# Kernel optimization log

Hardware: AMD Instinct MI355X
Metric: run time of the kernel (lower is better)

## Reference

```python
import jax, jax.numpy as jnp
import numpy as np


def setup_inputs() -> dict:
    key = jax.random.key(0)
    k1, k2, k3 = jax.random.split(key, 3)
    N, C, Nf, W, H = 8, 256, 16, 28, 28
    l = jax.random.normal(k1, (N, C, Nf, W, H), dtype=jnp.float32)
    g = jax.random.normal(k2, (N, C, 1, 1, 1), dtype=jnp.float32)
    # 1x1x1 Conv3d(in=C, out=1, bias=False) weight collapses to a length-C vector
    w = jax.random.normal(k3, (C,), dtype=jnp.float32) * (1.0 / np.sqrt(C))
    return {"l": l, "g": g, "w": w}


def reference(l, g, w):
    # l: [N,C,Nf,W,H], g broadcastable to l, w: [C]
    N, C, Nf, W, H = l.shape
    # compatibility score: channel dot-product (1x1x1 conv, out_channels=1)
    c = jnp.einsum('ncfwh,c->nfwh', l + g, w)                      # [N,Nf,W,H]
    # softmax over the spatial dims (W*H) per frame, normalize_attn=True
    a = jax.nn.softmax(c.reshape(N, Nf, W * H), axis=-1)           # [N,Nf,WH]
    a = a.reshape(N, Nf, W, H)
    # attention-weighted spatial sum pooling -> [N,C,Nf]
    g_out = jnp.einsum('nfwh,ncfwh->ncf', a, l)
    # module returns raw compatibility map (pre-softmax) squeezed, and pooled g
    return (c, g_out)
```

## Files before the change

### kernel.cpp

```cpp
#include <hip/hip_runtime.h>
#include <math.h>

constexpr int N_ = 8, C_ = 256, F_ = 16, WH_ = 784;
constexpr int CH_STRIDE = F_ * WH_;
constexpr int COUT_SZ = N_ * F_ * WH_;
constexpr int QP = 196;
constexpr int TILE = 28;
constexpr int NT = 7;
constexpr int LSTR = 36;
constexpr int F4PT = TILE / 4;
constexpr int SOFF = 512 * C_;

__device__ inline float wave_reduce_sum(float v) {
#pragma unroll
  for (int o = 32; o > 0; o >>= 1) v += __shfl_down(v, o, 64);
  return v;
}

__global__ __launch_bounds__(1024, 8) void fused_kernel(
    const float* __restrict__ l, const float* __restrict__ g,
    const float* __restrict__ w, float* __restrict__ out,
    float* __restrict__ ws) {
  __shared__ float buf[C_ * LSTR];
  __shared__ float w_s[C_];
  __shared__ float e_s[TILE];
  __shared__ float red_s[16];
  __shared__ float gb_s;

  const int bid = blockIdx.x;
  const int nf = bid >> 2, qh = bid & 3;
  const int n = nf >> 4, f = nf & 15;
  const int tid = threadIdx.x;
  const int lane = tid & 63, wv = tid >> 6;

  if (tid < C_) w_s[tid] = w[tid];
  float gv = (tid < C_) ? g[n * C_ + tid] * w[tid] : 0.f;
  gv = wave_reduce_sum(gv);
  if (lane == 0) red_s[wv] = gv;
  __syncthreads();
  if (tid == 0) {
    float s = 0.f;
#pragma unroll
    for (int i = 0; i < 16; ++i) s += red_s[i];
    gb_s = s;
  }
  __syncthreads();
  const float gb = gb_s;

  const int idx0 = tid;
  const int c0s = idx0 / F4PT, j0 = idx0 - c0s * F4PT;
  const int og0 = c0s * CH_STRIDE + (j0 << 2);
  const int ol0 = c0s * LSTR + (j0 << 2);
  const int idx1 = 1024 + tid;
  const int c1s = idx1 / F4PT, j1 = idx1 - c1s * F4PT;
  const int og1 = c1s * CH_STRIDE + (j1 << 2);
  const int ol1 = c1s * LSTR + (j1 << 2);
  const bool a1 = (tid < 768);
  const size_t gbase =
      (size_t)n * (C_ * CH_STRIDE) + (size_t)f * WH_ + qh * QP;

  const int p16 = tid >> 4, s16 = tid & 15;
  const int gc = tid >> 2, q = tid & 3;

  float gacc = 0.f;
  float s_part = 0.f;

  for (int t = 0; t < NT; ++t) {
    {
      const float* lp = l + gbase + t * TILE;
      const float4 v0 = *reinterpret_cast<const float4*>(lp + og0);
      if (a1) {
        const float4 v1 = *reinterpret_cast<const float4*>(lp + og1);
        *reinterpret_cast<float4*>(&buf[ol1]) = v1;
      }
      *reinterpret_cast<float4*>(&buf[ol0]) = v0;
    }
    __syncthreads();

    if (tid < TILE * 16) {
      float acc = 0.f;
#pragma unroll
      for (int k = 0; k < 16; ++k) {
        const int c = s16 + (k << 4);
        acc = fmaf(buf[c * LSTR + p16], w_s[c], acc);
      }
      acc += __shfl_down(acc, 8, 64);
      acc += __shfl_down(acc, 4, 64);
      acc += __shfl_down(acc, 2, 64);
      acc += __shfl_down(acc, 1, 64);
      if (s16 == 0) {
        const float cp = acc + gb;
        out[nf * WH_ + qh * QP + t * TILE + p16] = cp;
        const float e = __expf(cp);
        e_s[p16] = e;
        s_part += e;
      }
    }
    __syncthreads();

    {
      const int pb = q * 7;
#pragma unroll
      for (int j = 0; j < 7; ++j)
        gacc = fmaf(buf[gc * LSTR + pb + j], e_s[pb + j], gacc);
    }
    __syncthreads();
  }

  gacc += __shfl_down(gacc, 2, 64);
  gacc += __shfl_down(gacc, 1, 64);
  if (q == 0) ws[bid * C_ + gc] = gacc;

  float sp = wave_reduce_sum(s_part);
  if (lane == 0) red_s[wv] = sp;
  __syncthreads();
  if (tid == 0) {
    float ssum = 0.f;
#pragma unroll
    for (int i = 0; i < 16; ++i) ssum += red_s[i];
    ws[SOFF + bid] = ssum;
  }
}

__global__ __launch_bounds__(1024) void combine_kernel(
    float* __restrict__ out, const float* __restrict__ ws) {
  const int tg = blockIdx.x * 1024 + threadIdx.x;
  const int nf = tg >> 8, c = tg & 255;
  const int n = nf >> 4, f = nf & 15;
  const int b0 = nf << 2;
  const float G = ws[(b0 + 0) * C_ + c] + ws[(b0 + 1) * C_ + c] +
                  ws[(b0 + 2) * C_ + c] + ws[(b0 + 3) * C_ + c];
  const float S = ws[SOFF + b0] + ws[SOFF + b0 + 1] +
                  ws[SOFF + b0 + 2] + ws[SOFF + b0 + 3];
  out[COUT_SZ + (size_t)(n * C_ + c) * F_ + f] = G / S;
}

extern "C" void kernel_launch(void* const* d_in, const int* in_sizes, int n_in,
                              void* d_out, int out_size, void* d_ws,
                              size_t ws_size, hipStream_t stream) {
  const float* l = (const float*)d_in[0];
  const float* g = (const float*)d_in[1];
  const float* w = (const float*)d_in[2];
  float* out = (float*)d_out;
  float* ws = (float*)d_ws;
  fused_kernel<<<dim3(4 * N_ * F_), dim3(1024), 0, stream>>>(l, g, w, out, ws);
  combine_kernel<<<dim3(32), dim3(1024), 0, stream>>>(out, ws);
}
```

Measured before the change: 160.6 us.

## Double-buffer tiles with asynchronous global-to-LDS loads

Replaces the register-staged global-to-shared copy with `__builtin_amdgcn_global_load_lds` direct-to-LDS loads into two unpadded tile buffers. The next tile is prefetched while the current one is being reduced, so global memory latency overlaps with compute instead of stalling every iteration. The first tile is issued before the `g`·`w` bias reduction so that latency is hidden too. One barrier is replaced by a manual waitcnt plus barrier. In exchange the kernel uses more LDS and drops the row padding. Correctness now depends on the DMA writes being complete before the barrier that follows them.

```diff
diff --git a/kernel.cpp b/kernel.cpp
--- a/kernel.cpp
+++ b/kernel.cpp
@@ -7,8 +7,8 @@
 constexpr int QP = 196;
 constexpr int TILE = 28;
 constexpr int NT = 7;
-constexpr int LSTR = 36;
 constexpr int F4PT = TILE / 4;
+constexpr int TILE_F = C_ * TILE;
 constexpr int SOFF = 512 * C_;
 
 __device__ inline float wave_reduce_sum(float v) {
@@ -17,11 +17,18 @@
   return v;
 }
 
+__device__ inline void gload16(const float* gp, float* lp) {
+  __builtin_amdgcn_global_load_lds(
+      (const __attribute__((address_space(1))) void*)gp,
+      (__attribute__((address_space(3))) void*)lp, 16, 0, 0);
+}
+
 __global__ __launch_bounds__(1024, 8) void fused_kernel(
     const float* __restrict__ l, const float* __restrict__ g,
     const float* __restrict__ w, float* __restrict__ out,
     float* __restrict__ ws) {
-  __shared__ float buf[C_ * LSTR];
+  __shared__ float bufA[TILE_F];
+  __shared__ float bufB[TILE_F];
   __shared__ float w_s[C_];
   __shared__ float e_s[TILE];
   __shared__ float red_s[16];
@@ -32,6 +39,23 @@
   const int n = nf >> 4, f = nf & 15;
   const int tid = threadIdx.x;
   const int lane = tid & 63, wv = tid >> 6;
+
+  const int c0 = tid / F4PT, j0 = tid - c0 * F4PT;
+  const int og0 = c0 * CH_STRIDE + (j0 << 2);
+  const int idx1 = 1024 + tid;
+  const int c1 = idx1 / F4PT, j1 = idx1 - c1 * F4PT;
+  const int og1 = c1 * CH_STRIDE + (j1 << 2);
+  const bool a1 = (tid < 768);
+  const int l0 = wv << 8;
+  const int l1 = 4096 + (wv << 8);
+  const size_t gbase =
+      (size_t)n * (C_ * CH_STRIDE) + (size_t)f * WH_ + qh * QP;
+
+  {
+    const float* lp = l + gbase;
+    gload16(lp + og0, &bufA[l0]);
+    if (a1) gload16(lp + og1, &bufA[l1]);
+  }
 
   if (tid < C_) w_s[tid] = w[tid];
   float gv = (tid < C_) ? g[n * C_ + tid] * w[tid] : 0.f;
@@ -47,42 +71,27 @@
   __syncthreads();
   const float gb = gb_s;
 
-  const int idx0 = tid;
-  const int c0s = idx0 / F4PT, j0 = idx0 - c0s * F4PT;
-  const int og0 = c0s * CH_STRIDE + (j0 << 2);
-  const int ol0 = c0s * LSTR + (j0 << 2);
-  const int idx1 = 1024 + tid;
-  const int c1s = idx1 / F4PT, j1 = idx1 - c1s * F4PT;
-  const int og1 = c1s * CH_STRIDE + (j1 << 2);
-  const int ol1 = c1s * LSTR + (j1 << 2);
-  const bool a1 = (tid < 768);
-  const size_t gbase =
-      (size_t)n * (C_ * CH_STRIDE) + (size_t)f * WH_ + qh * QP;
-
   const int p16 = tid >> 4, s16 = tid & 15;
   const int gc = tid >> 2, q = tid & 3;
 
+  float* cur = bufA;
+  float* nxt = bufB;
   float gacc = 0.f;
   float s_part = 0.f;
 
   for (int t = 0; t < NT; ++t) {
-    {
-      const float* lp = l + gbase + t * TILE;
-      const float4 v0 = *reinterpret_cast<const float4*>(lp + og0);
-      if (a1) {
-        const float4 v1 = *reinterpret_cast<const float4*>(lp + og1);
-        *reinterpret_cast<float4*>(&buf[ol1]) = v1;
-      }
-      *reinterpret_cast<float4*>(&buf[ol0]) = v0;
+    if (t + 1 < NT) {
+      const float* lp = l + gbase + (t + 1) * TILE;
+      gload16(lp + og0, &nxt[l0]);
+      if (a1) gload16(lp + og1, &nxt[l1]);
     }
-    __syncthreads();
 
     if (tid < TILE * 16) {
       float acc = 0.f;
 #pragma unroll
       for (int k = 0; k < 16; ++k) {
         const int c = s16 + (k << 4);
-        acc = fmaf(buf[c * LSTR + p16], w_s[c], acc);
+        acc = fmaf(cur[c * TILE + p16], w_s[c], acc);
       }
       acc += __shfl_down(acc, 8, 64);
       acc += __shfl_down(acc, 4, 64);
@@ -96,15 +105,19 @@
         s_part += e;
       }
     }
-    __syncthreads();
+    asm volatile("s_waitcnt lgkmcnt(0)" ::: "memory");
+    __builtin_amdgcn_s_barrier();
+    __builtin_amdgcn_sched_barrier(0);
 
     {
       const int pb = q * 7;
 #pragma unroll
       for (int j = 0; j < 7; ++j)
-        gacc = fmaf(buf[gc * LSTR + pb + j], e_s[pb + j], gacc);
+        gacc = fmaf(cur[gc * TILE + pb + j], e_s[pb + j], gacc);
     }
     __syncthreads();
+
+    float* tmp = cur; cur = nxt; nxt = tmp;
   }
 
   gacc += __shfl_down(gacc, 2, 64);
```

After: 159.6 us. Within noise of the previous version (-0.6%).
